# Kernel optimization log

Measured on AMD Instinct MI355X. Metric: run time of the kernel, lower is better.

## Reference

```python
import jax, jax.numpy as jnp
import numpy as np

MIN_C = 1e-5   # base_c * DYNAMIC_CURVATURE_MIN_RATIO
MAX_C = 10.0   # base_c * DYNAMIC_CURVATURE_MAX_RATIO
T = 0.7
EPS = 1e-7
B, IN_DIM, HID, OUT_DIM = 4096, 4096, 4096, 1024


def _artanh(x):
    x = jnp.clip(x, -1.0 + 1e-5, 1.0 - 1e-5)
    return 0.5 * jnp.log1p(2.0 * x / (1.0 - x))


def _mobius_scalar_mul(r, x, c):
    # r: python float, x: [B,D], c: [B,1] per-row curvature
    sqrt_c = jnp.sqrt(c)
    norm = jnp.clip(jnp.linalg.norm(x, axis=-1, keepdims=True), EPS)
    arg = jnp.clip(sqrt_c * norm, EPS, 1.0 - 1e-5)
    return jnp.tanh(r * _artanh(arg)) * x / (sqrt_c * norm)


def _mobius_add(x, y, c):
    xy = jnp.sum(x * y, axis=-1, keepdims=True)
    x2 = jnp.sum(x * x, axis=-1, keepdims=True)
    y2 = jnp.sum(y * y, axis=-1, keepdims=True)
    num = (1.0 + 2.0 * c * xy + c * y2) * x + (1.0 - c * x2) * y
    den = 1.0 + 2.0 * c * xy + c * c * x2 * y2
    return num / jnp.clip(den, EPS)


def poincare_ball_layer(h, u, c, t):
    # geodesic-style layer: ((1-t) (*) h) (+) (t (*) u) on the Poincare ball
    return _mobius_add(_mobius_scalar_mul(1.0 - t, h, c),
                       _mobius_scalar_mul(t, u, c), c)


def setup_inputs() -> dict:
    key = jax.random.key(0)
    ks = jax.random.split(key, 8)
    std = 0.02  # WEIGHT_INIT_STD_IMPROVED
    return {
        "x": jax.random.normal(ks[0], (B, IN_DIM), jnp.float32),
        "W1": jax.random.normal(ks[1], (IN_DIM, HID), jnp.float32) * std,
        "b1": jnp.zeros((HID,), jnp.float32),
        "W2": jax.random.normal(ks[2], (HID, HID), jnp.float32) * std,
        "b2": jnp.zeros((HID,), jnp.float32),
        "Wout": jax.random.normal(ks[3], (HID, OUT_DIM), jnp.float32) * std,
        "bout": jnp.zeros((OUT_DIM,), jnp.float32),
        "curv_feat": jax.random.normal(ks[4], (16,), jnp.float32) * 0.01,
        "curv_scale": jnp.ones((1,), jnp.float32) * 0.1,
        "proj": jax.random.normal(ks[5], (IN_DIM, 16), jnp.float32),
    }


def reference(x, W1, b1, W2, b2, Wout, bout, curv_feat, curv_scale, proj):
    x_flat = x.reshape(x.shape[0], -1)
    h = jnp.tanh(x_flat @ W1 + b1)            # [B, HID]
    u = jax.nn.sigmoid(h @ W2 + b2)           # [B, HID]
    # adaptive curvature prediction (vectorized over batch)
    x_red = x_flat @ proj                     # [B, 16]
    feat_inter = x_red @ curv_feat            # [B]
    adj = jax.nn.sigmoid(feat_inter + curv_scale[0])
    c = MIN_C + (MAX_C - MIN_C) * adj         # [B]
    c = jnp.clip(c, MIN_C, MAX_C)[:, None]    # [B, 1]
    z = poincare_ball_layer(h, u, c, T)
    # NaN fallback per row (mirrors torch per-sample isnan check)
    z = jnp.where(jnp.any(jnp.isnan(z), axis=1, keepdims=True), h, z)
    return z @ Wout + bout
```

## Files before the change

kernel.cpp:

```cpp
#include <hip/hip_runtime.h>
#include <hip/hip_bf16.h>
#include <math.h>


typedef __attribute__((ext_vector_type(8))) __bf16 bf16x8;
typedef __attribute__((ext_vector_type(4))) float  f32x4;

constexpr int BATCH = 4096;
constexpr int IND   = 4096;
constexpr int HIDD  = 4096;
constexpr int OUTD  = 1024;
constexpr float T_C  = 0.7f;
constexpr float MINC = 1e-5f;
constexpr float MAXC = 10.0f;
constexpr float EPSV = 1e-7f;

__device__ __forceinline__ float bf2f(unsigned int us) {
    return __uint_as_float(us << 16);
}
__device__ __forceinline__ unsigned short f2bf(float f) {
    unsigned int u = __float_as_uint(f);
    u = (u + 0x7FFFu + ((u >> 16) & 1u)) >> 16;
    return (unsigned short)u;
}

__global__ __launch_bounds__(256)
void cast_f32_bf16(const float* __restrict__ in, unsigned short* __restrict__ out, int n)
{
    const int n4 = n >> 2;
    for (int j = blockIdx.x * 256 + threadIdx.x; j < n4; j += gridDim.x * 256) {
        float4 v = ((const float4*)in)[j];
        ushort4 o;
        o.x = f2bf(v.x); o.y = f2bf(v.y); o.z = f2bf(v.z); o.w = f2bf(v.w);
        ((ushort4*)out)[j] = o;
    }
}

__global__ __launch_bounds__(256)
void transpose_cast(const float* __restrict__ in, unsigned short* __restrict__ out,
                    int K, int N)
{
    __shared__ float tile[32][33];
    const int k0 = blockIdx.y * 32;
    const int n0 = blockIdx.x * 32;
    const int t = threadIdx.x;
    #pragma unroll
    for (int i = 0; i < 4; i++) {
        int idx = t + i * 256;
        int r = idx >> 5, c = idx & 31;
        tile[r][c] = in[(size_t)(k0 + r) * N + n0 + c];
    }
    __syncthreads();
    #pragma unroll
    for (int i = 0; i < 4; i++) {
        int idx = t + i * 256;
        int r = idx >> 5, c = idx & 31;
        out[(size_t)(n0 + r) * K + k0 + c] = f2bf(tile[c][r]);
    }
}

template<int EPI>
__global__ __launch_bounds__(512)
void gemm256(const unsigned short* __restrict__ A,
             const unsigned short* __restrict__ Bt,
             const float* __restrict__ bias,
             unsigned short* __restrict__ outp,
             int N, int K)
{
    __shared__ unsigned short lds[4 * 256 * 64];
    unsigned short* Al = lds;
    unsigned short* Bl = lds + 2 * 256 * 64;

    const int t = threadIdx.x;
    const int w = t >> 6, l = t & 63;
    const int wr = w >> 2, wc = w & 3;
    const int lr = l & 15, lg = l >> 4;

    const int nwg = gridDim.x * gridDim.y;
    const int bid = blockIdx.y * gridDim.x + blockIdx.x;
    const int q8 = nwg >> 3, r8 = nwg & 7;
    const int xcd = bid & 7, off = bid >> 3;
    const int wgid = (xcd < r8 ? xcd * (q8 + 1) : r8 * (q8 + 1) + (xcd - r8) * q8) + off;
    const int by = wgid / gridDim.x;
    const int bx = wgid % gridDim.x;

    const int row0 = by * 256, col0 = bx * 256;
    const unsigned short* Ab = A  + (size_t)row0 * K;
    const unsigned short* Bb = Bt + (size_t)col0 * K;
    const int NT = K >> 6;

    f32x4 acc[8][4] = {};

    auto stage = [&](int kt, int buf) {
        const int kb = kt * 128;
        #pragma unroll
        for (int s = 0; s < 8; s++) {
            const int mat = s >> 2;
            const int h   = (s >> 1) & 1;
            const int qq  = s & 1;
            const int id  = qq * 512 + t;
            const int row = h * 128 + (id >> 3);
            const int cb  = (id & 7) * 16;
            const int scb = cb ^ ((row & 7) << 4);
            const char* src = (const char*)(mat ? Bb : Ab)
                            + (size_t)row * ((size_t)K * 2) + kb + scb;
            unsigned short* dst = (mat ? Bl : Al) + buf * 16384 + h * 8192 + id * 8;
            __builtin_amdgcn_global_load_lds(
                (const __attribute__((address_space(1))) unsigned int*)src,
                (__attribute__((address_space(3))) unsigned int*)dst, 16, 0, 0);
        }
    };

    stage(0, 0);
    asm volatile("s_waitcnt vmcnt(0)" ::: "memory");
    __builtin_amdgcn_s_barrier();

    const int sw = (lr & 7) << 4;
    for (int kt = 0; kt < NT; ++kt) {
        const int buf = kt & 1;
        if (kt + 1 < NT) stage(kt + 1, buf ^ 1);

        const char* AlB = (const char*)Al + buf * 32768 + (wr * 128 + lr) * 128;
        const char* BlB = (const char*)Bl + buf * 32768 + (wc * 64 + lr) * 128;
        const int c0 = (lg * 16) ^ sw;
        const int c1 = (64 + lg * 16) ^ sw;

        bf16x8 bf[4][2];
        #pragma unroll
        for (int ni = 0; ni < 4; ni++) {
            bf[ni][0] = *(const bf16x8*)(BlB + ni * 2048 + c0);
            bf[ni][1] = *(const bf16x8*)(BlB + ni * 2048 + c1);
        }

        #pragma unroll
        for (int p = 0; p < 4; p++) {
            bf16x8 af[2][2];
            #pragma unroll
            for (int ms = 0; ms < 2; ms++) {
                af[ms][0] = *(const bf16x8*)(AlB + (2 * p + ms) * 2048 + c0);
                af[ms][1] = *(const bf16x8*)(AlB + (2 * p + ms) * 2048 + c1);
            }
            __builtin_amdgcn_s_setprio(1);
            #pragma unroll
            for (int ms = 0; ms < 2; ms++)
                #pragma unroll
                for (int ni = 0; ni < 4; ni++) {
                    acc[2 * p + ms][ni] = __builtin_amdgcn_mfma_f32_16x16x32_bf16(
                        af[ms][0], bf[ni][0], acc[2 * p + ms][ni], 0, 0, 0);
                    acc[2 * p + ms][ni] = __builtin_amdgcn_mfma_f32_16x16x32_bf16(
                        af[ms][1], bf[ni][1], acc[2 * p + ms][ni], 0, 0, 0);
                }
            __builtin_amdgcn_s_setprio(0);
            if (p < 3) __builtin_amdgcn_s_barrier();
        }
        asm volatile("s_waitcnt vmcnt(0)" ::: "memory");
        __builtin_amdgcn_s_barrier();
    }

    const int colb = col0 + wc * 64;
    const int rowb = row0 + wr * 128 + lg * 4;
    #pragma unroll
    for (int ni = 0; ni < 4; ni++) {
        const int cg = colb + ni * 16 + lr;
        const float bv = bias[cg];
        #pragma unroll
        for (int mi = 0; mi < 8; mi++) {
            #pragma unroll
            for (int r = 0; r < 4; r++) {
                const int rg = rowb + mi * 16 + r;
                float v = acc[mi][ni][r] + bv;
                if constexpr (EPI == 0) v = tanhf(v);
                else                    v = 1.0f / (1.0f + expf(-v));
                outp[(size_t)rg * N + cg] = f2bf(v);
            }
        }
    }
}

__global__ __launch_bounds__(256)
void gemm_bt_f32(const unsigned short* __restrict__ A,
                 const unsigned short* __restrict__ Bt,
                 const float* __restrict__ bias,
                 float* __restrict__ outp,
                 int N, int K)
{
    __shared__ unsigned short Asl[128 * 32];
    __shared__ unsigned short Bsl[128 * 32];

    const int t  = threadIdx.x;
    const int w  = t >> 6, l = t & 63;
    const int wr = w >> 1, wc = w & 1;
    const int row0 = blockIdx.y * 128;
    const int col0 = blockIdx.x * 128;

    const unsigned short* Ab = A  + (size_t)row0 * K;
    const unsigned short* Bb = Bt + (size_t)col0 * K;

    const int lr = l & 15;
    const int lk = (l >> 4) * 8;

    f32x4 acc[4][4] = {};

    for (int k0 = 0; k0 < K; k0 += 32) {
        __syncthreads();
        #pragma unroll
        for (int q = 0; q < 2; q++) {
            int idx = q * 256 + t;
            int r   = idx >> 2;
            int c8  = (idx & 3) * 8;
            __builtin_amdgcn_global_load_lds(
                (const __attribute__((address_space(1))) unsigned int*)(Ab + (size_t)r * K + k0 + c8),
                (__attribute__((address_space(3))) unsigned int*)(&Asl[idx * 8]), 16, 0, 0);
            __builtin_amdgcn_global_load_lds(
                (const __attribute__((address_space(1))) unsigned int*)(Bb + (size_t)r * K + k0 + c8),
                (__attribute__((address_space(3))) unsigned int*)(&Bsl[idx * 8]), 16, 0, 0);
        }
        __syncthreads();

        bf16x8 af[4], bfr[4];
        #pragma unroll
        for (int mi = 0; mi < 4; mi++)
            af[mi] = *(const bf16x8*)(&Asl[(wr * 64 + mi * 16 + lr) * 32 + lk]);
        #pragma unroll
        for (int ni = 0; ni < 4; ni++)
            bfr[ni] = *(const bf16x8*)(&Bsl[(wc * 64 + ni * 16 + lr) * 32 + lk]);

        #pragma unroll
        for (int mi = 0; mi < 4; mi++)
            #pragma unroll
            for (int ni = 0; ni < 4; ni++)
                acc[mi][ni] = __builtin_amdgcn_mfma_f32_16x16x32_bf16(
                    af[mi], bfr[ni], acc[mi][ni], 0, 0, 0);
    }

    const int colb = col0 + wc * 64;
    const int rowb = row0 + wr * 64 + (l >> 4) * 4;
    #pragma unroll
    for (int ni = 0; ni < 4; ni++) {
        const int cg = colb + ni * 16 + lr;
        const float bv = bias[cg];
        #pragma unroll
        for (int mi = 0; mi < 4; mi++)
            #pragma unroll
            for (int r = 0; r < 4; r++)
                outp[(size_t)(rowb + mi * 16 + r) * N + cg] = acc[mi][ni][r] + bv;
    }
}

__global__ __launch_bounds__(256)
void proj_cf(const float* __restrict__ proj, const float* __restrict__ cf,
             float* __restrict__ v)
{
    int i = blockIdx.x * 256 + threadIdx.x;
    if (i < IND) {
        float s = 0.f;
        #pragma unroll
        for (int j = 0; j < 16; j++) s += proj[i * 16 + j] * cf[j];
        v[i] = s;
    }
}

__global__ __launch_bounds__(256)
void curv_kernel(const float* __restrict__ x, const float* __restrict__ v,
                 const float* __restrict__ cs, float* __restrict__ c)
{
    const int row = blockIdx.x;
    const float* xr = x + (size_t)row * IND;
    float s = 0.f;
    for (int j = threadIdx.x; j < IND; j += 256) s += xr[j] * v[j];
    #pragma unroll
    for (int o = 32; o > 0; o >>= 1) s += __shfl_down(s, o, 64);
    __shared__ float red[4];
    if ((threadIdx.x & 63) == 0) red[threadIdx.x >> 6] = s;
    __syncthreads();
    if (threadIdx.x == 0) {
        float tot = red[0] + red[1] + red[2] + red[3];
        float adj = 1.0f / (1.0f + expf(-(tot + cs[0])));
        float cc  = MINC + (MAXC - MINC) * adj;
        c[row] = fminf(fmaxf(cc, MINC), MAXC);
    }
}

__global__ __launch_bounds__(256)
void poincare_kernel(const unsigned short* __restrict__ hb,
                     const unsigned short* __restrict__ ub,
                     const float* __restrict__ c,
                     unsigned short* __restrict__ zb)
{
    const int row = blockIdx.x;
    const int t = threadIdx.x;
    const size_t base = (size_t)row * HIDD;

    float hv[16], uv[16];
    float h2 = 0.f, u2 = 0.f, hu = 0.f;
    #pragma unroll
    for (int q = 0; q < 2; q++) {
        const int e0 = (q * 256 + t) * 8;
        uint4 hc = *(const uint4*)(hb + base + e0);
        uint4 uc = *(const uint4*)(ub + base + e0);
        const unsigned int hw[4] = {hc.x, hc.y, hc.z, hc.w};
        const unsigned int uw[4] = {uc.x, uc.y, uc.z, uc.w};
        #pragma unroll
        for (int i = 0; i < 4; i++) {
            float h0 = bf2f(hw[i] & 0xFFFFu), h1 = bf2f(hw[i] >> 16);
            float u0 = bf2f(uw[i] & 0xFFFFu), u1 = bf2f(uw[i] >> 16);
            hv[q * 8 + 2 * i]     = h0; hv[q * 8 + 2 * i + 1] = h1;
            uv[q * 8 + 2 * i]     = u0; uv[q * 8 + 2 * i + 1] = u1;
            h2 += h0 * h0 + h1 * h1;
            u2 += u0 * u0 + u1 * u1;
            hu += h0 * u0 + h1 * u1;
        }
    }
    #pragma unroll
    for (int o = 32; o > 0; o >>= 1) {
        h2 += __shfl_down(h2, o, 64);
        u2 += __shfl_down(u2, o, 64);
        hu += __shfl_down(hu, o, 64);
    }
    __shared__ float red[3][4];
    const int w = t >> 6;
    if ((t & 63) == 0) { red[0][w] = h2; red[1][w] = u2; red[2][w] = hu; }
    __syncthreads();
    h2 = red[0][0] + red[0][1] + red[0][2] + red[0][3];
    u2 = red[1][0] + red[1][1] + red[1][2] + red[1][3];
    hu = red[2][0] + red[2][1] + red[2][2] + red[2][3];

    const float cc = c[row];
    const float sc = sqrtf(cc);
    float nh = fmaxf(sqrtf(h2), EPSV);
    float nu = fmaxf(sqrtf(u2), EPSV);
    float ah = fminf(fmaxf(sc * nh, EPSV), 1.0f - 1e-5f);
    float au = fminf(fmaxf(sc * nu, EPSV), 1.0f - 1e-5f);
    float ath = 0.5f * log1pf(2.0f * ah / (1.0f - ah));
    float atu = 0.5f * log1pf(2.0f * au / (1.0f - au));
    float alpha = tanhf((1.0f - T_C) * ath) / (sc * nh);
    float beta  = tanhf(T_C * atu) / (sc * nu);
    float x2 = alpha * alpha * h2;
    float y2 = beta * beta * u2;
    float xy = alpha * beta * hu;
    float den = 1.0f + 2.0f * cc * xy + cc * cc * x2 * y2;
    den = fmaxf(den, EPSV);
    float ca = (1.0f + 2.0f * cc * xy + cc * y2) * alpha / den;
    float cb = (1.0f - cc * x2) * beta / den;
    if (isnan(ca) || isnan(cb)) { ca = 1.0f; cb = 0.0f; }

    #pragma unroll
    for (int q = 0; q < 2; q++) {
        const int e0 = (q * 256 + t) * 8;
        unsigned int ow[4];
        #pragma unroll
        for (int i = 0; i < 4; i++) {
            float z0 = ca * hv[q * 8 + 2 * i]     + cb * uv[q * 8 + 2 * i];
            float z1 = ca * hv[q * 8 + 2 * i + 1] + cb * uv[q * 8 + 2 * i + 1];
            ow[i] = (unsigned int)f2bf(z0) | ((unsigned int)f2bf(z1) << 16);
        }
        *(uint4*)(zb + base + e0) = make_uint4(ow[0], ow[1], ow[2], ow[3]);
    }
}

extern "C" void kernel_launch(void* const* d_in, const int* in_sizes, int n_in,
                              void* d_out, int out_size, void* d_ws, size_t ws_size,
                              hipStream_t stream)
{
    const float* x    = (const float*)d_in[0];
    const float* W1   = (const float*)d_in[1];
    const float* b1   = (const float*)d_in[2];
    const float* W2   = (const float*)d_in[3];
    const float* b2   = (const float*)d_in[4];
    const float* Wout = (const float*)d_in[5];
    const float* bout = (const float*)d_in[6];
    const float* cf   = (const float*)d_in[7];
    const float* cs   = (const float*)d_in[8];
    const float* proj = (const float*)d_in[9];
    float* out = (float*)d_out;

    char* ws = (char*)d_ws;
    unsigned short* x_bf = (unsigned short*)(ws);
    unsigned short* w_bf = (unsigned short*)(ws + (33554432));
    unsigned short* h_bf = (unsigned short*)(ws + (67108864));
    unsigned short* u_bf = (unsigned short*)(ws + (100663296));
    float* vvec = (float*)(ws + 134217728);
    float* cvec = (float*)(ws + 134217728 + 16384);

    cast_f32_bf16<<<2048, 256, 0, stream>>>(x, x_bf, BATCH * IND);
    proj_cf<<<IND / 256, 256, 0, stream>>>(proj, cf, vvec);
    curv_kernel<<<BATCH, 256, 0, stream>>>(x, vvec, cs, cvec);

    transpose_cast<<<dim3(HIDD / 32, IND / 32), 256, 0, stream>>>(W1, w_bf, IND, HIDD);
    gemm256<0><<<dim3(HIDD / 256, BATCH / 256), 512, 0, stream>>>(x_bf, w_bf, b1, h_bf, HIDD, IND);

    transpose_cast<<<dim3(HIDD / 32, HIDD / 32), 256, 0, stream>>>(W2, w_bf, HIDD, HIDD);
    gemm256<1><<<dim3(HIDD / 256, BATCH / 256), 512, 0, stream>>>(h_bf, w_bf, b2, u_bf, HIDD, HIDD);

    poincare_kernel<<<BATCH, 256, 0, stream>>>(h_bf, u_bf, cvec, x_bf);

    transpose_cast<<<dim3(OUTD / 32, HIDD / 32), 256, 0, stream>>>(Wout, w_bf, HIDD, OUTD);
    gemm_bt_f32<<<dim3(OUTD / 128, BATCH / 128), 256, 0, stream>>>(x_bf, w_bf, bout, out, OUTD, HIDD);
}
```

Measured before the change: 453.2 us.

## Fuse x cast with curvature reduction and interleave GEMM prefetch into compute phases

The fp32-to-bf16 cast of x is merged with the per-row curvature dot product, so x is read from global memory once instead of twice. In the 256x256 bf16 GEMM, the next K-tile's global-to-LDS loads are split into four quarter-stages issued between the MFMA phases, with partial vmcnt waits in place of one bulk load and full drain per iteration. The warp-to-row mapping is interleaved (wr*16 + mi*32) so each phase's A rows line up with the quarter just loaded. This aims to hide load latency behind MFMA work, but the finer waits and a barrier after every phase add synchronisation and ordering risk.

```diff
diff --git a/kernel.cpp b/kernel.cpp
--- a/kernel.cpp
+++ b/kernel.cpp
@@ -25,14 +25,32 @@
 }
 
 __global__ __launch_bounds__(256)
-void cast_f32_bf16(const float* __restrict__ in, unsigned short* __restrict__ out, int n)
-{
-    const int n4 = n >> 2;
-    for (int j = blockIdx.x * 256 + threadIdx.x; j < n4; j += gridDim.x * 256) {
-        float4 v = ((const float4*)in)[j];
+void cast_curv(const float* __restrict__ x, const float* __restrict__ v,
+               const float* __restrict__ cs,
+               unsigned short* __restrict__ xb, float* __restrict__ c)
+{
+    const int row = blockIdx.x;
+    const float* xr = x + (size_t)row * IND;
+    unsigned short* ob = xb + (size_t)row * IND;
+    float s = 0.f;
+    for (int i = threadIdx.x; i < IND / 4; i += 256) {
+        float4 w  = ((const float4*)xr)[i];
+        float4 vv = ((const float4*)v)[i];
+        s += w.x * vv.x + w.y * vv.y + w.z * vv.z + w.w * vv.w;
         ushort4 o;
-        o.x = f2bf(v.x); o.y = f2bf(v.y); o.z = f2bf(v.z); o.w = f2bf(v.w);
-        ((ushort4*)out)[j] = o;
+        o.x = f2bf(w.x); o.y = f2bf(w.y); o.z = f2bf(w.z); o.w = f2bf(w.w);
+        ((ushort4*)ob)[i] = o;
+    }
+    #pragma unroll
+    for (int o = 32; o > 0; o >>= 1) s += __shfl_down(s, o, 64);
+    __shared__ float red[4];
+    if ((threadIdx.x & 63) == 0) red[threadIdx.x >> 6] = s;
+    __syncthreads();
+    if (threadIdx.x == 0) {
+        float tot = red[0] + red[1] + red[2] + red[3];
+        float adj = 1.0f / (1.0f + expf(-(tot + cs[0])));
+        float cc  = MINC + (MAXC - MINC) * adj;
+        c[row] = fminf(fmaxf(cc, MINC), MAXC);
     }
 }
 
@@ -91,54 +109,59 @@
 
     f32x4 acc[8][4] = {};
 
-    auto stage = [&](int kt, int buf) {
+    auto stage_half = [&](int kt, int buf, int mat, int h) {
         const int kb = kt * 128;
-        #pragma unroll
-        for (int s = 0; s < 8; s++) {
-            const int mat = s >> 2;
-            const int h   = (s >> 1) & 1;
-            const int qq  = s & 1;
+        const unsigned short* gb = mat ? Bb : Ab;
+        unsigned short* lb = (mat ? Bl : Al) + buf * 16384 + h * 8192;
+        #pragma unroll
+        for (int qq = 0; qq < 2; qq++) {
             const int id  = qq * 512 + t;
             const int row = h * 128 + (id >> 3);
             const int cb  = (id & 7) * 16;
             const int scb = cb ^ ((row & 7) << 4);
-            const char* src = (const char*)(mat ? Bb : Ab)
-                            + (size_t)row * ((size_t)K * 2) + kb + scb;
-            unsigned short* dst = (mat ? Bl : Al) + buf * 16384 + h * 8192 + id * 8;
+            const char* src = (const char*)gb + (size_t)row * ((size_t)K * 2) + kb + scb;
             __builtin_amdgcn_global_load_lds(
                 (const __attribute__((address_space(1))) unsigned int*)src,
-                (__attribute__((address_space(3))) unsigned int*)dst, 16, 0, 0);
+                (__attribute__((address_space(3))) unsigned int*)(lb + id * 8), 16, 0, 0);
         }
     };
 
-    stage(0, 0);
-    asm volatile("s_waitcnt vmcnt(0)" ::: "memory");
+    stage_half(0, 0, 0, 0);
+    stage_half(0, 0, 1, 0);
+    stage_half(0, 0, 1, 1);
+    stage_half(0, 0, 0, 1);
+    asm volatile("s_waitcnt vmcnt(2)" ::: "memory");
     __builtin_amdgcn_s_barrier();
 
     const int sw = (lr & 7) << 4;
+    const int c0 = (lg * 16) ^ sw;
+    const int c1 = (64 + lg * 16) ^ sw;
+
     for (int kt = 0; kt < NT; ++kt) {
-        const int buf = kt & 1;
-        if (kt + 1 < NT) stage(kt + 1, buf ^ 1);
-
-        const char* AlB = (const char*)Al + buf * 32768 + (wr * 128 + lr) * 128;
+        const int buf = kt & 1, nb = buf ^ 1;
+        const bool pre = (kt + 1 < NT);
+        const char* AlB = (const char*)Al + buf * 32768 + (wr * 16 + lr) * 128;
         const char* BlB = (const char*)Bl + buf * 32768 + (wc * 64 + lr) * 128;
-        const int c0 = (lg * 16) ^ sw;
-        const int c1 = (64 + lg * 16) ^ sw;
-
-        bf16x8 bf[4][2];
+
+        bf16x8 bfr[4][2];
         #pragma unroll
         for (int ni = 0; ni < 4; ni++) {
-            bf[ni][0] = *(const bf16x8*)(BlB + ni * 2048 + c0);
-            bf[ni][1] = *(const bf16x8*)(BlB + ni * 2048 + c1);
-        }
-
+            bfr[ni][0] = *(const bf16x8*)(BlB + ni * 2048 + c0);
+            bfr[ni][1] = *(const bf16x8*)(BlB + ni * 2048 + c1);
+        }
         #pragma unroll
         for (int p = 0; p < 4; p++) {
             bf16x8 af[2][2];
             #pragma unroll
             for (int ms = 0; ms < 2; ms++) {
-                af[ms][0] = *(const bf16x8*)(AlB + (2 * p + ms) * 2048 + c0);
-                af[ms][1] = *(const bf16x8*)(AlB + (2 * p + ms) * 2048 + c1);
+                af[ms][0] = *(const bf16x8*)(AlB + (size_t)(2 * p + ms) * 4096 + c0);
+                af[ms][1] = *(const bf16x8*)(AlB + (size_t)(2 * p + ms) * 4096 + c1);
+            }
+            if (pre) {
+                if (p == 0)      stage_half(kt + 1, nb, 0, 0);
+                else if (p == 1) stage_half(kt + 1, nb, 1, 0);
+                else if (p == 2) stage_half(kt + 1, nb, 1, 1);
+                else             stage_half(kt + 1, nb, 0, 1);
             }
             __builtin_amdgcn_s_setprio(1);
             #pragma unroll
@@ -146,19 +169,23 @@
                 #pragma unroll
                 for (int ni = 0; ni < 4; ni++) {
                     acc[2 * p + ms][ni] = __builtin_amdgcn_mfma_f32_16x16x32_bf16(
-                        af[ms][0], bf[ni][0], acc[2 * p + ms][ni], 0, 0, 0);
+                        af[ms][0], bfr[ni][0], acc[2 * p + ms][ni], 0, 0, 0);
                     acc[2 * p + ms][ni] = __builtin_amdgcn_mfma_f32_16x16x32_bf16(
-                        af[ms][1], bf[ni][1], acc[2 * p + ms][ni], 0, 0, 0);
+                        af[ms][1], bfr[ni][1], acc[2 * p + ms][ni], 0, 0, 0);
                 }
             __builtin_amdgcn_s_setprio(0);
-            if (p < 3) __builtin_amdgcn_s_barrier();
-        }
-        asm volatile("s_waitcnt vmcnt(0)" ::: "memory");
-        __builtin_amdgcn_s_barrier();
+            if (p == 1) {
+                if (pre) asm volatile("s_waitcnt vmcnt(4)" ::: "memory");
+                else     asm volatile("s_waitcnt vmcnt(0)" ::: "memory");
+            } else if (p == 3) {
+                if (pre) asm volatile("s_waitcnt vmcnt(2)" ::: "memory");
+                else     asm volatile("s_waitcnt vmcnt(0)" ::: "memory");
+            }
+            __builtin_amdgcn_s_barrier();
+        }
     }
 
     const int colb = col0 + wc * 64;
-    const int rowb = row0 + wr * 128 + lg * 4;
     #pragma unroll
     for (int ni = 0; ni < 4; ni++) {
         const int cg = colb + ni * 16 + lr;
@@ -167,7 +194,7 @@
         for (int mi = 0; mi < 8; mi++) {
             #pragma unroll
             for (int r = 0; r < 4; r++) {
-                const int rg = rowb + mi * 16 + r;
+                const int rg = row0 + wr * 16 + mi * 32 + lg * 4 + r;
                 float v = acc[mi][ni][r] + bv;
                 if constexpr (EPI == 0) v = tanhf(v);
                 else                    v = 1.0f / (1.0f + expf(-v));
@@ -257,27 +284,6 @@
         #pragma unroll
         for (int j = 0; j < 16; j++) s += proj[i * 16 + j] * cf[j];
         v[i] = s;
-    }
-}
-
-__global__ __launch_bounds__(256)
-void curv_kernel(const float* __restrict__ x, const float* __restrict__ v,
-                 const float* __restrict__ cs, float* __restrict__ c)
-{
-    const int row = blockIdx.x;
-    const float* xr = x + (size_t)row * IND;
-    float s = 0.f;
-    for (int j = threadIdx.x; j < IND; j += 256) s += xr[j] * v[j];
-    #pragma unroll
-    for (int o = 32; o > 0; o >>= 1) s += __shfl_down(s, o, 64);
-    __shared__ float red[4];
-    if ((threadIdx.x & 63) == 0) red[threadIdx.x >> 6] = s;
-    __syncthreads();
-    if (threadIdx.x == 0) {
-        float tot = red[0] + red[1] + red[2] + red[3];
-        float adj = 1.0f / (1.0f + expf(-(tot + cs[0])));
-        float cc  = MINC + (MAXC - MINC) * adj;
-        c[row] = fminf(fmaxf(cc, MINC), MAXC);
     }
 }
 
@@ -382,9 +388,8 @@
     float* vvec = (float*)(ws + 134217728);
     float* cvec = (float*)(ws + 134217728 + 16384);
 
-    cast_f32_bf16<<<2048, 256, 0, stream>>>(x, x_bf, BATCH * IND);
     proj_cf<<<IND / 256, 256, 0, stream>>>(proj, cf, vvec);
-    curv_kernel<<<BATCH, 256, 0, stream>>>(x, vvec, cs, cvec);
+    cast_curv<<<BATCH, 256, 0, stream>>>(x, vvec, cs, x_bf, cvec);
 
     transpose_cast<<<dim3(HIDD / 32, IND / 32), 256, 0, stream>>>(W1, w_bf, IND, HIDD);
     gemm256<0><<<dim3(HIDD / 256, BATCH / 256), 512, 0, stream>>>(x_bf, w_bf, b1, h_bf, HIDD, IND);
```

Result: faster. 433.1 us (-4.4%).
